# Optimization experiments

Hardware: AMD Instinct MI355X
Metric: run time of the kernel (lower is better)

## Reference

```python
import jax, jax.numpy as jnp
import numpy as np

N = 26000       # total nodes (1040 graphs * 25 joints)
E = 208000      # total edges
G = 1040        # graphs (16 samples * 65 frames)
FRAMES = 65
F_IN = 6
HID = 128
HEADS = 4
NCLS = 7


def setup_inputs() -> dict:
    key = jax.random.key(0)
    ks = jax.random.split(key, 30)

    def nrm(k, shape, s=0.05):
        return jax.random.normal(k, shape, dtype=jnp.float32) * s

    return {
        "x": jax.random.normal(ks[0], (N, F_IN), dtype=jnp.float32),
        "edge_index": jax.random.randint(ks[1], (2, E), 0, N, dtype=jnp.int32),
        "batch": jnp.arange(N, dtype=jnp.int32) // (N // G),  # 25 nodes per graph
        "w1_root": nrm(ks[2], (F_IN, HID)),
        "w1_nei": nrm(ks[3], (F_IN, HID)),
        "b1": nrm(ks[4], (HID,)),
        "wq": nrm(ks[5], (HID, HEADS * HID)),
        "bq": nrm(ks[6], (HEADS * HID,)),
        "wk": nrm(ks[7], (HID, HEADS * HID)),
        "bk": nrm(ks[8], (HEADS * HID,)),
        "wv": nrm(ks[9], (HID, HEADS * HID)),
        "bv": nrm(ks[10], (HEADS * HID,)),
        "wskip": nrm(ks[11], (HID, HEADS * HID)),
        "bskip": nrm(ks[12], (HEADS * HID,)),
        "skip_w": nrm(ks[13], (HID, HEADS * HID)),
        "lin1_w": nrm(ks[14], (HEADS * HID, HID)),
        "lin1_b": nrm(ks[15], (HID,)),
        "l2_root": nrm(ks[16], (HID, HID)),
        "l2_nei": nrm(ks[17], (HID, HID)),
        "l2_b": nrm(ks[18], (HID,)),
        "l3_root": nrm(ks[19], (HID, HID)),
        "l3_nei": nrm(ks[20], (HID, HID)),
        "l3_b": nrm(ks[21], (HID,)),
        "fc_w": nrm(ks[22], (HID, NCLS)),
        "fc_b": nrm(ks[23], (NCLS,)),
    }


def _graph_conv(x, src, dst, w_root, w_nei, b):
    # PyG GraphConv (aggr='add'): W_root x_i + W_nei * sum_{j in N(i)} x_j + b
    agg = jax.ops.segment_sum(x[src], dst, num_segments=N)
    return x @ w_root + agg @ w_nei + b


def _transformer_conv(x, src, dst, wq, bq, wk, bk, wv, bv, wskip, bskip):
    # PyG TransformerConv, concat=True, root_weight=True, beta=False.
    # Dropout on attention is inference-disabled.
    q = (x @ wq + bq).reshape(N, HEADS, HID)
    k = (x @ wk + bk).reshape(N, HEADS, HID)
    v = (x @ wv + bv).reshape(N, HEADS, HID)
    logits = jnp.einsum('ehc,ehc->eh', q[dst], k[src]) / jnp.sqrt(jnp.float32(HID))
    m = jax.ops.segment_max(logits, dst, num_segments=N)          # [N,H]
    a = jnp.exp(logits - m[dst])                                  # [E,H]
    denom = jax.ops.segment_sum(a, dst, num_segments=N)           # [N,H]
    num = jax.ops.segment_sum(a[:, :, None] * v[src], dst, num_segments=N)  # [N,H,C]
    out = num / jnp.where(denom == 0, 1.0, denom)[:, :, None]
    return out.reshape(N, HEADS * HID) + (x @ wskip + bskip)


def reference(x, edge_index, batch,
              w1_root, w1_nei, b1,
              wq, bq, wk, bk, wv, bv, wskip, bskip,
              skip_w, lin1_w, lin1_b,
              l2_root, l2_nei, l2_b,
              l3_root, l3_nei, l3_b,
              fc_w, fc_b):
    src, dst = edge_index[0], edge_index[1]
    h = jax.nn.relu(_graph_conv(x, src, dst, w1_root, w1_nei, b1))
    skip_out = h @ skip_w  # external skip Linear (no bias)
    h = jax.nn.relu(_transformer_conv(h, src, dst, wq, bq, wk, bk, wv, bv, wskip, bskip) + skip_out)
    h = jax.nn.relu(h @ lin1_w + lin1_b)
    for wr, wn, b in ((l2_root, l2_nei, l2_b), (l3_root, l3_nei, l3_b)):
        h = jax.nn.relu(_graph_conv(h, src, dst, wr, wn, b) + h)
    # global_mean_pool over graphs
    sums = jax.ops.segment_sum(h, batch, num_segments=G)
    cnts = jax.ops.segment_sum(jnp.ones((N,), jnp.float32), batch, num_segments=G)
    pooled = sums / jnp.where(cnts == 0, 1.0, cnts)[:, None]      # [G, HID]
    # average over 65 frames per sample, then classify
    z = pooled.reshape(-1, FRAMES, HID).mean(axis=1)              # [G/65, HID]
    return z @ fc_w + fc_b
```

## Files before the change

### kernel.cpp

```cpp
#include <hip/hip_runtime.h>
#include <math.h>

#define NN 26000
#define NE 208000
#define SCAN_CH 26
#define CNT_BLOCKS 813

typedef __attribute__((ext_vector_type(8))) short bf16x8;
typedef __attribute__((ext_vector_type(4))) float f32x4;
typedef __attribute__((ext_vector_type(2))) float f32x2;
typedef unsigned char u8;

__device__ __forceinline__ float bf2f(ushort u){
  union { unsigned int i; float f; } w; w.i = ((unsigned int)u) << 16; return w.f;
}
__device__ __forceinline__ ushort f2bf(float f){
  union { float f; unsigned int i; } w; w.f = f;
  unsigned int u = w.i + 0x7fffu + ((w.i >> 16) & 1u);
  return (ushort)(u >> 16);
}

__global__ void cp_k(const int* __restrict__ dst, int* __restrict__ cnt,
                     const float* __restrict__ wq, const float* __restrict__ wk,
                     const float* __restrict__ wv, const float* __restrict__ wskip,
                     const float* __restrict__ skw, const float* __restrict__ lin1w,
                     const float* __restrict__ l2r, const float* __restrict__ l2n,
                     const float* __restrict__ l3r, const float* __restrict__ l3n,
                     ushort* __restrict__ wbuf){
  if (blockIdx.x < CNT_BLOCKS){
    int e = blockIdx.x*256 + threadIdx.x;
    if (e < NE) atomicAdd(&cnt[dst[e]], 1);
    return;
  }
  int idx = (blockIdx.x - CNT_BLOCKS)*256 + threadIdx.x;
  if (idx >= 393216) return;
  float v;
  if (idx < 262144){
    int seg = idx >> 16;
    int local = idx & 65535;
    int n = local >> 7, kk = local & 127;
    const float* w = (seg == 0) ? wq : (seg == 1) ? wk : (seg == 2) ? wv : wskip;
    v = w[kk*512 + n];
    if (seg == 3) v += skw[kk*512 + n];
  } else if (idx < 327680){
    int local = idx - 262144;
    int n = local >> 9, kk = local & 511;
    v = lin1w[kk*128 + n];
  } else {
    int rem = idx - 327680;
    int seg = rem >> 14;
    int local = rem & 16383;
    int n = local >> 7, kk = local & 127;
    const float* w = (seg == 0) ? l2r : (seg == 1) ? l2n : (seg == 2) ? l3r : l3n;
    v = w[kk*128 + n];
  }
  wbuf[idx] = f2bf(v);
}

__global__ __launch_bounds__(1024) void scan_k(int* __restrict__ cnt_cur, int* __restrict__ off){
  int t = threadIdx.x;
  int base = t * SCAN_CH;
  int v[SCAN_CH];
  #pragma unroll
  for (int j = 0; j < SCAN_CH; ++j){
    int idx = base + j;
    v[j] = (idx < NN) ? cnt_cur[idx] : 0;
  }
  int s = 0;
  #pragma unroll
  for (int j = 0; j < SCAN_CH; ++j) s += v[j];
  __shared__ int ls[1024];
  ls[t] = s; __syncthreads();
  for (int ofs = 1; ofs < 1024; ofs <<= 1){
    int u = (t >= ofs) ? ls[t - ofs] : 0;
    __syncthreads();
    ls[t] += u;
    __syncthreads();
  }
  int run = (t == 0) ? 0 : ls[t-1];
  #pragma unroll
  for (int j = 0; j < SCAN_CH; ++j){
    int idx = base + j;
    if (idx < NN){
      off[idx] = run;
      cnt_cur[idx] = run;
      run += v[j];
    }
  }
  if (t == 1023) off[NN] = ls[1023];
}

__global__ void fill_k(const int* __restrict__ src, const int* __restrict__ dst,
                       int* __restrict__ cur, int* __restrict__ csrc, int E){
  int e = blockIdx.x*256 + threadIdx.x;
  if (e < E){
    int p = atomicAdd(&cur[dst[e]], 1);
    csrc[p] = src[e];
  }
}

__global__ __launch_bounds__(256) void layer1_k(
    const float* __restrict__ x, const int* __restrict__ off,
    const int* __restrict__ csrc, const float* __restrict__ w1r,
    const float* __restrict__ w1n, const float* __restrict__ b1,
    ushort* __restrict__ h1)
{
  __shared__ float aggs[2][6];
  int slot = threadIdx.x >> 7, c = threadIdx.x & 127;
  int i = blockIdx.x*2 + slot;
  if (c < 6){
    float s = 0.f;
    int e1 = off[i+1];
    for (int j = off[i]; j < e1; ++j) s += x[(size_t)csrc[j]*6 + c];
    aggs[slot][c] = s;
  }
  __syncthreads();
  float s = b1[c];
  #pragma unroll
  for (int f = 0; f < 6; ++f){
    s = fmaf(x[i*6+f],    w1r[f*128+c], s);
    s = fmaf(aggs[slot][f], w1n[f*128+c], s);
  }
  h1[(size_t)i*128 + c] = f2bf(fmaxf(s, 0.f));
}

__global__ __launch_bounds__(256) void qkvs_k(
    const ushort* __restrict__ A, const ushort* __restrict__ BT,
    const float* __restrict__ bq, const float* __restrict__ bk,
    const float* __restrict__ bv, const float* __restrict__ bs,
    u8* __restrict__ cq, u8* __restrict__ ckv,
    ushort* __restrict__ cs, int M)
{
  __shared__ ushort smem[2*128*72];
  ushort* Asm = smem;
  ushort* Bsm = smem + 128*72;
  int tid  = threadIdx.x;
  int lane = tid & 63;
  int wid  = tid >> 6;
  int wr = wid >> 1, wc = wid & 1;
  int rowbase = blockIdx.y * 128;
  int seg = blockIdx.x >> 2;
  const float* bias = (seg == 0) ? bq : (seg == 1) ? bk : (seg == 2) ? bv : bs;
  int colloc = (blockIdx.x & 3) * 128;
  int lr = lane & 15, lk = (lane >> 4) * 8;

  f32x4 acc[4][4] = {};

  for (int k0 = 0; k0 < 128; k0 += 64){
    #pragma unroll
    for (int i = 0; i < 4; ++i){
      int c = tid + i*256;
      int r = c >> 3, col8 = (c & 7) * 8;
      int row = rowbase + r;
      bf16x8 av = (bf16x8)0;
      if (row < M) av = *reinterpret_cast<const bf16x8*>(A + (size_t)row*128 + k0 + col8);
      *reinterpret_cast<bf16x8*>(&Asm[r*72 + col8]) = av;
      *reinterpret_cast<bf16x8*>(&Bsm[r*72 + col8]) =
          *reinterpret_cast<const bf16x8*>(BT + (size_t)(blockIdx.x*128 + r)*128 + k0 + col8);
    }
    __syncthreads();
    #pragma unroll
    for (int ks = 0; ks < 64; ks += 32){
      bf16x8 af[4], bfr[4];
      #pragma unroll
      for (int i = 0; i < 4; ++i)
        af[i] = *reinterpret_cast<const bf16x8*>(&Asm[(wr*64 + i*16 + lr)*72 + ks + lk]);
      #pragma unroll
      for (int j = 0; j < 4; ++j)
        bfr[j] = *reinterpret_cast<const bf16x8*>(&Bsm[(wc*64 + j*16 + lr)*72 + ks + lk]);
      #pragma unroll
      for (int i = 0; i < 4; ++i)
        #pragma unroll
        for (int j = 0; j < 4; ++j)
          acc[i][j] = __builtin_amdgcn_mfma_f32_16x16x32_bf16(af[i], bfr[j], acc[i][j], 0, 0, 0);
    }
    __syncthreads();
  }

  int rq = lane >> 4;
  #pragma unroll
  for (int i = 0; i < 4; ++i)
    #pragma unroll
    for (int r = 0; r < 4; ++r){
      int lrow = wr*64 + i*16 + rq*4 + r;
      #pragma unroll
      for (int j = 0; j < 4; ++j){
        int lcol = wc*64 + j*16 + lr;
        smem[lrow*136 + lcol] = f2bf(acc[i][j][r] + bias[colloc + lcol]);
      }
    }
  __syncthreads();

  if (seg <= 2){
    u8* Cb; int ldb, cb;
    if (seg == 0){ Cb = cq;  ldb = 512;  cb = colloc; }
    else         { Cb = ckv; ldb = 1024; cb = (seg == 1 ? 0 : 512) + colloc; }
    #pragma unroll
    for (int t = tid; t < 2048; t += 256){
      int r = t >> 4, s8 = (t & 15) * 8;
      int row = rowbase + r;
      if (row < M){
        bf16x8 hv = *reinterpret_cast<const bf16x8*>(&smem[r*136 + s8]);
        unsigned int lo = 0, hi = 0;
        lo = __builtin_amdgcn_cvt_pk_fp8_f32(bf2f((ushort)hv[0]), bf2f((ushort)hv[1]), lo, false);
        lo = __builtin_amdgcn_cvt_pk_fp8_f32(bf2f((ushort)hv[2]), bf2f((ushort)hv[3]), lo, true);
        hi = __builtin_amdgcn_cvt_pk_fp8_f32(bf2f((ushort)hv[4]), bf2f((ushort)hv[5]), hi, false);
        hi = __builtin_amdgcn_cvt_pk_fp8_f32(bf2f((ushort)hv[6]), bf2f((ushort)hv[7]), hi, true);
        uint2 o; o.x = lo; o.y = hi;
        *reinterpret_cast<uint2*>(Cb + (size_t)row*ldb + cb + s8) = o;
      }
    }
  } else {
    #pragma unroll
    for (int t = tid; t < 2048; t += 256){
      int r = t >> 4, s8 = (t & 15) * 8;
      int row = rowbase + r;
      if (row < M)
        *reinterpret_cast<bf16x8*>(cs + (size_t)row*512 + colloc + s8) =
            *reinterpret_cast<const bf16x8*>(&smem[r*136 + s8]);
    }
  }
}

__global__ __launch_bounds__(256) void bgemm64_k(
    const ushort* __restrict__ A1, int lda1, const ushort* __restrict__ B1T, int K1,
    const float* __restrict__ bias, ushort* __restrict__ C, int M, int N)
{
  __shared__ ushort As[64][72];
  __shared__ ushort Bs[128][72];
  int tid  = threadIdx.x;
  int lane = tid & 63;
  int wid  = tid >> 6;
  int wr = wid >> 1, wc = wid & 1;
  int rowbase = blockIdx.y * 64;
  int colbase = blockIdx.x * 128;
  int lr = lane & 15, lk = (lane >> 4) * 8;

  f32x4 acc[2][4] = {};

  for (int k0 = 0; k0 < K1; k0 += 64){
    #pragma unroll
    for (int i = 0; i < 2; ++i){
      int c = tid + i*256;
      int r = c >> 3, col8 = (c & 7) * 8;
      int row = rowbase + r;
      bf16x8 av = (bf16x8)0;
      if (row < M) av = *reinterpret_cast<const bf16x8*>(A1 + (size_t)row*lda1 + k0 + col8);
      *reinterpret_cast<bf16x8*>(&As[r][col8]) = av;
    }
    #pragma unroll
    for (int i = 0; i < 4; ++i){
      int c = tid + i*256;
      int r = c >> 3, col8 = (c & 7) * 8;
      *reinterpret_cast<bf16x8*>(&Bs[r][col8]) =
          *reinterpret_cast<const bf16x8*>(B1T + (size_t)(colbase + r)*K1 + k0 + col8);
    }
    __syncthreads();
    #pragma unroll
    for (int ks = 0; ks < 64; ks += 32){
      bf16x8 af[2], bfr[4];
      #pragma unroll
      for (int i = 0; i < 2; ++i)
        af[i] = *reinterpret_cast<const bf16x8*>(&As[wr*32 + i*16 + lr][ks + lk]);
      #pragma unroll
      for (int j = 0; j < 4; ++j)
        bfr[j] = *reinterpret_cast<const bf16x8*>(&Bs[wc*64 + j*16 + lr][ks + lk]);
      #pragma unroll
      for (int i = 0; i < 2; ++i)
        #pragma unroll
        for (int j = 0; j < 4; ++j)
          acc[i][j] = __builtin_amdgcn_mfma_f32_16x16x32_bf16(af[i], bfr[j], acc[i][j], 0, 0, 0);
    }
    __syncthreads();
  }

  int rq = lane >> 4;
  #pragma unroll
  for (int i = 0; i < 2; ++i){
    #pragma unroll
    for (int r = 0; r < 4; ++r){
      int row = rowbase + wr*32 + i*16 + rq*4 + r;
      if (row >= M) continue;
      #pragma unroll
      for (int j = 0; j < 4; ++j){
        int col = colbase + wc*64 + j*16 + lr;
        if (col >= N) continue;
        float v = fmaxf(acc[i][j][r] + bias[col], 0.f);
        C[(size_t)row*N + col] = f2bf(v);
      }
    }
  }
}

__global__ __launch_bounds__(256) void gconv_k(
    const ushort* __restrict__ h, const ushort* __restrict__ WrT,
    const ushort* __restrict__ WnT, const float* __restrict__ bias,
    const int* __restrict__ off, const int* __restrict__ csrc,
    ushort* __restrict__ out, int M)
{
  __shared__ ushort As1[64][136];
  __shared__ ushort As2[64][136];
  int tid = threadIdx.x, lane = tid & 63, wid = tid >> 6;
  int wr = wid >> 1, wc = wid & 1;
  int rowbase = blockIdx.x * 64;
  int lr = lane & 15, lk = (lane >> 4) * 8;

  #pragma unroll
  for (int it = 0; it < 4; ++it){
    int c = tid + it*256;
    int r = c >> 4, col8 = (c & 15) * 8;
    int row = rowbase + r;
    bf16x8 av = (bf16x8)0;
    if (row < M) av = *reinterpret_cast<const bf16x8*>(h + (size_t)row*128 + col8);
    *reinterpret_cast<bf16x8*>(&As1[r][col8]) = av;
  }
  {
    int r = tid >> 2, sl = tid & 3;
    int row = rowbase + r;
    float a[32] = {};
    if (row < M){
      int e1 = off[row+1];
      for (int j = off[row]; j < e1; ++j){
        const ushort* hp = h + (size_t)csrc[j]*128 + sl*32;
        #pragma unroll
        for (int u = 0; u < 4; ++u){
          bf16x8 hv = *reinterpret_cast<const bf16x8*>(hp + u*8);
          #pragma unroll
          for (int p = 0; p < 8; ++p) a[u*8+p] += bf2f((ushort)hv[p]);
        }
      }
    }
    #pragma unroll
    for (int u = 0; u < 4; ++u){
      bf16x8 o;
      #pragma unroll
      for (int p = 0; p < 8; ++p) o[p] = (short)f2bf(a[u*8+p]);
      *reinterpret_cast<bf16x8*>(&As2[r][sl*32 + u*8]) = o;
    }
  }
  __syncthreads();

  f32x4 acc[2][4] = {};
  #pragma unroll
  for (int pass = 0; pass < 2; ++pass){
    const ushort* BT = pass ? WnT : WrT;
    #pragma unroll
    for (int kk = 0; kk < 128; kk += 32){
      bf16x8 af[2], bfr[4];
      #pragma unroll
      for (int i = 0; i < 2; ++i)
        af[i] = pass
          ? *reinterpret_cast<const bf16x8*>(&As2[wr*32 + i*16 + lr][kk + lk])
          : *reinterpret_cast<const bf16x8*>(&As1[wr*32 + i*16 + lr][kk + lk]);
      #pragma unroll
      for (int j = 0; j < 4; ++j)
        bfr[j] = *reinterpret_cast<const bf16x8*>(
            BT + (size_t)(wc*64 + j*16 + lr)*128 + kk + lk);
      #pragma unroll
      for (int i = 0; i < 2; ++i)
        #pragma unroll
        for (int j = 0; j < 4; ++j)
          acc[i][j] = __builtin_amdgcn_mfma_f32_16x16x32_bf16(af[i], bfr[j], acc[i][j], 0, 0, 0);
    }
  }

  int rq = lane >> 4;
  #pragma unroll
  for (int i = 0; i < 2; ++i){
    #pragma unroll
    for (int r = 0; r < 4; ++r){
      int lrow = wr*32 + i*16 + rq*4 + r;
      int row = rowbase + lrow;
      if (row >= M) continue;
      #pragma unroll
      for (int j = 0; j < 4; ++j){
        int col = wc*64 + j*16 + lr;
        float v = acc[i][j][r] + bias[col] + bf2f(As1[lrow][col]);
        out[(size_t)row*128 + col] = f2bf(fmaxf(v, 0.f));
      }
    }
  }
}

__global__ __launch_bounds__(256) void attn_k(
    const u8* __restrict__ q, const u8* __restrict__ kv,
    ushort* __restrict__ s_io,
    const int* __restrict__ off, const int* __restrict__ csrc)
{
  int lane = threadIdx.x & 63;
  int i = blockIdx.x*4 + (threadIdx.x >> 6);
  uint2 qv = *reinterpret_cast<const uint2*>(q + (size_t)i*512 + lane*8);
  f32x2 q01 = __builtin_amdgcn_cvt_pk_f32_fp8(qv.x, false);
  f32x2 q23 = __builtin_amdgcn_cvt_pk_f32_fp8(qv.x, true);
  f32x2 q45 = __builtin_amdgcn_cvt_pk_f32_fp8(qv.y, false);
  f32x2 q67 = __builtin_amdgcn_cvt_pk_f32_fp8(qv.y, true);
  float qf[8] = {q01[0], q01[1], q23[0], q23[1], q45[0], q45[1], q67[0], q67[1]};

  float d = 0.f, acc[8] = {};
  int e0 = off[i], e1 = off[i+1];
  uint2 kA, vA, kB, vB;
  if (e0 < e1){
    const u8* r = kv + (size_t)csrc[e0]*1024 + lane*8;
    kA = *reinterpret_cast<const uint2*>(r);
    vA = *reinterpret_cast<const uint2*>(r + 512);
  }
  if (e0 + 1 < e1){
    const u8* r = kv + (size_t)csrc[e0+1]*1024 + lane*8;
    kB = *reinterpret_cast<const uint2*>(r);
    vB = *reinterpret_cast<const uint2*>(r + 512);
  }
  for (int j = e0; j < e1; ++j){
    uint2 kc = kA, vc = vA;
    kA = kB; vA = vB;
    if (j + 2 < e1){
      const u8* r = kv + (size_t)csrc[j+2]*1024 + lane*8;
      kB = *reinterpret_cast<const uint2*>(r);
      vB = *reinterpret_cast<const uint2*>(r + 512);
    }
    f32x2 k01 = __builtin_amdgcn_cvt_pk_f32_fp8(kc.x, false);
    f32x2 k23 = __builtin_amdgcn_cvt_pk_f32_fp8(kc.x, true);
    f32x2 k45 = __builtin_amdgcn_cvt_pk_f32_fp8(kc.y, false);
    f32x2 k67 = __builtin_amdgcn_cvt_pk_f32_fp8(kc.y, true);
    float t;
    t = qf[0] * k01[0];
    t = fmaf(qf[1], k01[1], t);
    t = fmaf(qf[2], k23[0], t);
    t = fmaf(qf[3], k23[1], t);
    t = fmaf(qf[4], k45[0], t);
    t = fmaf(qf[5], k45[1], t);
    t = fmaf(qf[6], k67[0], t);
    t = fmaf(qf[7], k67[1], t);
    t += __shfl_xor(t, 1);
    t += __shfl_xor(t, 2);
    t += __shfl_xor(t, 4);
    t += __shfl_xor(t, 8);
    float w = __expf(t * 0.08838834764831845f);
    d += w;
    f32x2 v01 = __builtin_amdgcn_cvt_pk_f32_fp8(vc.x, false);
    f32x2 v23 = __builtin_amdgcn_cvt_pk_f32_fp8(vc.x, true);
    f32x2 v45 = __builtin_amdgcn_cvt_pk_f32_fp8(vc.y, false);
    f32x2 v67 = __builtin_amdgcn_cvt_pk_f32_fp8(vc.y, true);
    acc[0] = fmaf(w, v01[0], acc[0]);
    acc[1] = fmaf(w, v01[1], acc[1]);
    acc[2] = fmaf(w, v23[0], acc[2]);
    acc[3] = fmaf(w, v23[1], acc[3]);
    acc[4] = fmaf(w, v45[0], acc[4]);
    acc[5] = fmaf(w, v45[1], acc[5]);
    acc[6] = fmaf(w, v67[0], acc[6]);
    acc[7] = fmaf(w, v67[1], acc[7]);
  }
  float inv = (d > 0.f) ? 1.f/d : 0.f;
  ushort* rowp = s_io + (size_t)i*512 + lane*8;
  bf16x8 sk8 = *reinterpret_cast<const bf16x8*>(rowp);
  bf16x8 o8;
  #pragma unroll
  for (int p = 0; p < 8; ++p)
    o8[p] = (short)f2bf(fmaxf(bf2f((ushort)sk8[p]) + acc[p]*inv, 0.f));
  *reinterpret_cast<bf16x8*>(rowp) = o8;
}

__global__ __launch_bounds__(256) void fc1_k(const ushort* __restrict__ h,
                                             float* __restrict__ partial){
  int s = blockIdx.x, c0 = blockIdx.y;
  int t = threadIdx.x;
  int c = t & 127, g = t >> 7;
  float sum = 0.f;
  int rend = (c0 + 1) * 125;
  for (int r = c0*125 + g; r < rend; r += 2)
    sum += bf2f(h[((size_t)s*1625 + r)*128 + c]);
  __shared__ float zs[2][128];
  zs[g][c] = sum; __syncthreads();
  if (g == 0) partial[((size_t)s*13 + c0)*128 + c] = zs[0][c] + zs[1][c];
}

__global__ __launch_bounds__(128) void fc2_k(const float* __restrict__ partial,
    const float* __restrict__ fcw, const float* __restrict__ fcb,
    float* __restrict__ out)
{
  int s = blockIdx.x;
  int c = threadIdx.x;
  float z = 0.f;
  #pragma unroll
  for (int p = 0; p < 13; ++p) z += partial[((size_t)s*13 + p)*128 + c];
  __shared__ float zs[128];
  zs[c] = z * (1.0f/1625.0f);
  __syncthreads();
  if (c < 7){
    float o = fcb[c];
    for (int k2 = 0; k2 < 128; ++k2) o = fmaf(zs[k2], fcw[k2*7 + c], o);
    out[s*7 + c] = o;
  }
}

extern "C" void kernel_launch(void* const* d_in, const int* in_sizes, int n_in,
                              void* d_out, int out_size, void* d_ws, size_t ws_size,
                              hipStream_t stream)
{
  const float* x     = (const float*)d_in[0];
  const int*   ei    = (const int*)  d_in[1];
  const float* w1r   = (const float*)d_in[3];
  const float* w1n   = (const float*)d_in[4];
  const float* b1    = (const float*)d_in[5];
  const float* wq    = (const float*)d_in[6];
  const float* bq    = (const float*)d_in[7];
  const float* wk    = (const float*)d_in[8];
  const float* bk    = (const float*)d_in[9];
  const float* wv    = (const float*)d_in[10];
  const float* bv    = (const float*)d_in[11];
  const float* wskip = (const float*)d_in[12];
  const float* bskip = (const float*)d_in[13];
  const float* skw   = (const float*)d_in[14];
  const float* lin1w = (const float*)d_in[15];
  const float* lin1b = (const float*)d_in[16];
  const float* l2r   = (const float*)d_in[17];
  const float* l2n   = (const float*)d_in[18];
  const float* l2b   = (const float*)d_in[19];
  const float* l3r   = (const float*)d_in[20];
  const float* l3n   = (const float*)d_in[21];
  const float* l3b   = (const float*)d_in[22];
  const float* fcw   = (const float*)d_in[23];
  const float* fcb   = (const float*)d_in[24];
  float* out = (float*)d_out;

  const int* src = ei;
  const int* dst = ei + NE;

  char* base = (char*)d_ws;
  size_t o = 0;
  auto alloc = [&](size_t bytes) -> void* {
    o = (o + 255) & ~(size_t)255;
    void* p = base + o; o += bytes; return p;
  };
  int*    cnt     = (int*)   alloc((size_t)NN*4);
  int*    off     = (int*)   alloc((size_t)(NN+1)*4);
  int*    csrc    = (int*)   alloc((size_t)NE*4);
  float*  partial = (float*) alloc((size_t)16*13*128*4);
  ushort* h1      = (ushort*)alloc((size_t)NN*128*2);
  ushort* wbuf    = (ushort*)alloc((size_t)393216*2);
  u8*     bufQ8   = (u8*)    alloc((size_t)NN*512);
  u8*     bufKV   = (u8*)    alloc((size_t)NN*1024);
  ushort* bufS    = (ushort*)alloc((size_t)NN*512*2);
  ushort* hbuf    = (ushort*)alloc((size_t)NN*256*2);
  (void)ws_size; (void)in_sizes; (void)n_in; (void)out_size;

  const ushort* lin1T = wbuf + 262144;
  const ushort* l2rT  = wbuf + 327680;
  const ushort* l2nT  = wbuf + 344064;
  const ushort* l3rT  = wbuf + 360448;
  const ushort* l3nT  = wbuf + 376832;

  ushort* h3 = hbuf;
  ushort* h4 = hbuf + (size_t)NN*128;
  ushort* h5 = bufS;

  hipMemsetAsync(cnt, 0, (size_t)NN*4, stream);
  cp_k<<<CNT_BLOCKS + 1536, 256, 0, stream>>>(dst, cnt,
      wq, wk, wv, wskip, skw, lin1w, l2r, l2n, l3r, l3n, wbuf);
  scan_k<<<1, 1024, 0, stream>>>(cnt, off);
  fill_k<<<(NE+255)/256, 256, 0, stream>>>(src, dst, cnt, csrc, NE);

  layer1_k<<<NN/2, 256, 0, stream>>>(x, off, csrc, w1r, w1n, b1, h1);

  {
    dim3 g(16, (NN+127)/128);
    qkvs_k<<<g, 256, 0, stream>>>(h1, wbuf, bq, bk, bv, bskip,
                                  bufQ8, bufKV, bufS, NN);
  }

  attn_k<<<NN/4, 256, 0, stream>>>(bufQ8, bufKV, bufS, off, csrc);

  {
    dim3 g(1, (NN+63)/64);
    bgemm64_k<<<g, 256, 0, stream>>>(bufS, 512, lin1T, 512, lin1b, h3, NN, 128);
  }

  gconv_k<<<(NN+63)/64, 256, 0, stream>>>(h3, l2rT, l2nT, l2b, off, csrc, h4, NN);
  gconv_k<<<(NN+63)/64, 256, 0, stream>>>(h4, l3rT, l3nT, l3b, off, csrc, h5, NN);

  {
    dim3 g1(16, 13);
    fc1_k<<<g1, 256, 0, stream>>>(h5, partial);
    fc2_k<<<16, 128, 0, stream>>>(partial, fcw, fcb, out);
  }
}
```

Before: 287.6 us.

## Reuse A tile across four column tiles in QKVS GEMM, load B from global

The QKVS projection kernel now loads the full 128x128 A tile into shared memory once per block and loops over four 128-column output tiles, so the grid shrinks from 16 to 4 column blocks. This cuts the redundant reloads of A. B fragments are read directly from global memory (L2/L1) instead of being staged in LDS. The epilogue is split into two 64-row halves through a smaller staging buffer, and the launch bounds request 3 blocks per CU. The costs are fewer blocks and therefore less parallelism, uncoalesced-ish direct global B loads in the inner loop, and extra barriers in the epilogue.

```diff
diff --git a/kernel.cpp b/kernel.cpp
--- a/kernel.cpp
+++ b/kernel.cpp
@@ -124,100 +124,101 @@
   h1[(size_t)i*128 + c] = f2bf(fmaxf(s, 0.f));
 }
 
-__global__ __launch_bounds__(256) void qkvs_k(
+__global__ __launch_bounds__(256, 3) void qkvs_k(
     const ushort* __restrict__ A, const ushort* __restrict__ BT,
     const float* __restrict__ bq, const float* __restrict__ bk,
     const float* __restrict__ bv, const float* __restrict__ bs,
     u8* __restrict__ cq, u8* __restrict__ ckv,
     ushort* __restrict__ cs, int M)
 {
-  __shared__ ushort smem[2*128*72];
-  ushort* Asm = smem;
-  ushort* Bsm = smem + 128*72;
-  int tid  = threadIdx.x;
-  int lane = tid & 63;
-  int wid  = tid >> 6;
+  __shared__ ushort Asm[128*136];
+  __shared__ ushort epi[64*136];
+  int tid = threadIdx.x;
+  int lane = tid & 63, wid = tid >> 6;
   int wr = wid >> 1, wc = wid & 1;
+  int seg = blockIdx.x;
   int rowbase = blockIdx.y * 128;
-  int seg = blockIdx.x >> 2;
   const float* bias = (seg == 0) ? bq : (seg == 1) ? bk : (seg == 2) ? bv : bs;
-  int colloc = (blockIdx.x & 3) * 128;
   int lr = lane & 15, lk = (lane >> 4) * 8;
-
-  f32x4 acc[4][4] = {};
-
-  for (int k0 = 0; k0 < 128; k0 += 64){
-    #pragma unroll
-    for (int i = 0; i < 4; ++i){
-      int c = tid + i*256;
-      int r = c >> 3, col8 = (c & 7) * 8;
-      int row = rowbase + r;
-      bf16x8 av = (bf16x8)0;
-      if (row < M) av = *reinterpret_cast<const bf16x8*>(A + (size_t)row*128 + k0 + col8);
-      *reinterpret_cast<bf16x8*>(&Asm[r*72 + col8]) = av;
-      *reinterpret_cast<bf16x8*>(&Bsm[r*72 + col8]) =
-          *reinterpret_cast<const bf16x8*>(BT + (size_t)(blockIdx.x*128 + r)*128 + k0 + col8);
-    }
-    __syncthreads();
-    #pragma unroll
-    for (int ks = 0; ks < 64; ks += 32){
+  int rq = lane >> 4;
+
+  #pragma unroll
+  for (int it = 0; it < 8; ++it){
+    int c = tid + it*256;
+    int r = c >> 4, col8 = (c & 15) * 8;
+    int row = rowbase + r;
+    bf16x8 av = (bf16x8)0;
+    if (row < M) av = *reinterpret_cast<const bf16x8*>(A + (size_t)row*128 + col8);
+    *reinterpret_cast<bf16x8*>(&Asm[r*136 + col8]) = av;
+  }
+  __syncthreads();
+
+  for (int ct = 0; ct < 4; ++ct){
+    int colloc = ct * 128;
+    f32x4 acc[4][4] = {};
+    #pragma unroll
+    for (int kk = 0; kk < 128; kk += 32){
       bf16x8 af[4], bfr[4];
       #pragma unroll
       for (int i = 0; i < 4; ++i)
-        af[i] = *reinterpret_cast<const bf16x8*>(&Asm[(wr*64 + i*16 + lr)*72 + ks + lk]);
+        af[i] = *reinterpret_cast<const bf16x8*>(&Asm[(wr*64 + i*16 + lr)*136 + kk + lk]);
       #pragma unroll
       for (int j = 0; j < 4; ++j)
-        bfr[j] = *reinterpret_cast<const bf16x8*>(&Bsm[(wc*64 + j*16 + lr)*72 + ks + lk]);
+        bfr[j] = *reinterpret_cast<const bf16x8*>(
+            BT + (size_t)(seg*512 + colloc + wc*64 + j*16 + lr)*128 + kk + lk);
       #pragma unroll
       for (int i = 0; i < 4; ++i)
         #pragma unroll
         for (int j = 0; j < 4; ++j)
           acc[i][j] = __builtin_amdgcn_mfma_f32_16x16x32_bf16(af[i], bfr[j], acc[i][j], 0, 0, 0);
     }
-    __syncthreads();
-  }
-
-  int rq = lane >> 4;
-  #pragma unroll
-  for (int i = 0; i < 4; ++i)
-    #pragma unroll
-    for (int r = 0; r < 4; ++r){
-      int lrow = wr*64 + i*16 + rq*4 + r;
-      #pragma unroll
-      for (int j = 0; j < 4; ++j){
-        int lcol = wc*64 + j*16 + lr;
-        smem[lrow*136 + lcol] = f2bf(acc[i][j][r] + bias[colloc + lcol]);
+
+    #pragma unroll
+    for (int p = 0; p < 2; ++p){
+      __syncthreads();
+      if (wr == p){
+        #pragma unroll
+        for (int i = 0; i < 4; ++i)
+          #pragma unroll
+          for (int r = 0; r < 4; ++r){
+            int lrow = i*16 + rq*4 + r;
+            #pragma unroll
+            for (int j = 0; j < 4; ++j){
+              int lcol = wc*64 + j*16 + lr;
+              epi[lrow*136 + lcol] = f2bf(acc[i][j][r] + bias[colloc + lcol]);
+            }
+          }
       }
-    }
-  __syncthreads();
-
-  if (seg <= 2){
-    u8* Cb; int ldb, cb;
-    if (seg == 0){ Cb = cq;  ldb = 512;  cb = colloc; }
-    else         { Cb = ckv; ldb = 1024; cb = (seg == 1 ? 0 : 512) + colloc; }
-    #pragma unroll
-    for (int t = tid; t < 2048; t += 256){
-      int r = t >> 4, s8 = (t & 15) * 8;
-      int row = rowbase + r;
-      if (row < M){
-        bf16x8 hv = *reinterpret_cast<const bf16x8*>(&smem[r*136 + s8]);
-        unsigned int lo = 0, hi = 0;
-        lo = __builtin_amdgcn_cvt_pk_fp8_f32(bf2f((ushort)hv[0]), bf2f((ushort)hv[1]), lo, false);
-        lo = __builtin_amdgcn_cvt_pk_fp8_f32(bf2f((ushort)hv[2]), bf2f((ushort)hv[3]), lo, true);
-        hi = __builtin_amdgcn_cvt_pk_fp8_f32(bf2f((ushort)hv[4]), bf2f((ushort)hv[5]), hi, false);
-        hi = __builtin_amdgcn_cvt_pk_fp8_f32(bf2f((ushort)hv[6]), bf2f((ushort)hv[7]), hi, true);
-        uint2 o; o.x = lo; o.y = hi;
-        *reinterpret_cast<uint2*>(Cb + (size_t)row*ldb + cb + s8) = o;
+      __syncthreads();
+      if (seg <= 2){
+        u8* Cb; int ldb, cb;
+        if (seg == 0){ Cb = cq;  ldb = 512;  cb = colloc; }
+        else         { Cb = ckv; ldb = 1024; cb = (seg == 1 ? 0 : 512) + colloc; }
+        #pragma unroll
+        for (int t = tid; t < 1024; t += 256){
+          int r = t >> 4, s8 = (t & 15) * 8;
+          int row = rowbase + p*64 + r;
+          if (row < M){
+            bf16x8 hv = *reinterpret_cast<const bf16x8*>(&epi[r*136 + s8]);
+            unsigned int lo = 0, hi = 0;
+            lo = __builtin_amdgcn_cvt_pk_fp8_f32(bf2f((ushort)hv[0]), bf2f((ushort)hv[1]), lo, false);
+            lo = __builtin_amdgcn_cvt_pk_fp8_f32(bf2f((ushort)hv[2]), bf2f((ushort)hv[3]), lo, true);
+            hi = __builtin_amdgcn_cvt_pk_fp8_f32(bf2f((ushort)hv[4]), bf2f((ushort)hv[5]), hi, false);
+            hi = __builtin_amdgcn_cvt_pk_fp8_f32(bf2f((ushort)hv[6]), bf2f((ushort)hv[7]), hi, true);
+            uint2 o; o.x = lo; o.y = hi;
+            *reinterpret_cast<uint2*>(Cb + (size_t)row*ldb + cb + s8) = o;
+          }
+        }
+      } else {
+        #pragma unroll
+        for (int t = tid; t < 1024; t += 256){
+          int r = t >> 4, s8 = (t & 15) * 8;
+          int row = rowbase + p*64 + r;
+          if (row < M)
+            *reinterpret_cast<bf16x8*>(cs + (size_t)row*512 + colloc + s8) =
+                *reinterpret_cast<const bf16x8*>(&epi[r*136 + s8]);
+        }
       }
-    }
-  } else {
-    #pragma unroll
-    for (int t = tid; t < 2048; t += 256){
-      int r = t >> 4, s8 = (t & 15) * 8;
-      int row = rowbase + r;
-      if (row < M)
-        *reinterpret_cast<bf16x8*>(cs + (size_t)row*512 + colloc + s8) =
-            *reinterpret_cast<const bf16x8*>(&smem[r*136 + s8]);
     }
   }
 }
@@ -562,7 +563,7 @@
   layer1_k<<<NN/2, 256, 0, stream>>>(x, off, csrc, w1r, w1n, b1, h1);
 
   {
-    dim3 g(16, (NN+127)/128);
+    dim3 g(4, (NN+127)/128);
     qkvs_k<<<g, 256, 0, stream>>>(h1, wbuf, bq, bk, bv, bskip,
                                   bufQ8, bufKV, bufS, NN);
   }
```

New measurement: 311.2 us. 1.08x slower.

## Refactor attention algebraically: fold Wk into query side and apply Wv after aggregation

Applied to the files above, without the earlier changes.

Precomputes Wq·Wk^T per head and bq·Wk^T, so each node's query is projected into the 128-dim input space (u). Attention logits then become dot products of u with raw fp8 neighbour features h1 instead of gathered K rows, which shrinks per-edge gather traffic from 1 KB of K/V per edge to 128 bytes of h1. The key bias is dropped, which is exact because it adds the same constant to every logit of a destination node and cancels in the softmax. Values are aggregated in input space and the V projection is applied afterwards by a separate MFMA GEMM kernel, with bv scaled by a has-neighbours flag. This adds a kernel launch and a large bf16 aggregation buffer, and the fp8 quantisation of h1 and u may shift accuracy.

```diff
diff --git a/kernel.cpp b/kernel.cpp
--- a/kernel.cpp
+++ b/kernel.cpp
@@ -22,39 +22,67 @@
 
 __global__ void cp_k(const int* __restrict__ dst, int* __restrict__ cnt,
                      const float* __restrict__ wq, const float* __restrict__ wk,
-                     const float* __restrict__ wv, const float* __restrict__ wskip,
-                     const float* __restrict__ skw, const float* __restrict__ lin1w,
+                     const float* __restrict__ wv, const float* __restrict__ bq,
+                     const float* __restrict__ wskip, const float* __restrict__ skw,
+                     const float* __restrict__ lin1w,
                      const float* __restrict__ l2r, const float* __restrict__ l2n,
                      const float* __restrict__ l3r, const float* __restrict__ l3n,
-                     ushort* __restrict__ wbuf){
-  if (blockIdx.x < CNT_BLOCKS){
-    int e = blockIdx.x*256 + threadIdx.x;
+                     ushort* __restrict__ wbuf, float* __restrict__ bu){
+  int b = blockIdx.x, t = threadIdx.x;
+  if (b < CNT_BLOCKS){
+    int e = b*256 + t;
     if (e < NE) atomicAdd(&cnt[dst[e]], 1);
     return;
   }
-  int idx = (blockIdx.x - CNT_BLOCKS)*256 + threadIdx.x;
-  if (idx >= 393216) return;
-  float v;
-  if (idx < 262144){
-    int seg = idx >> 16;
-    int local = idx & 65535;
-    int n = local >> 7, kk = local & 127;
-    const float* w = (seg == 0) ? wq : (seg == 1) ? wk : (seg == 2) ? wv : wskip;
-    v = w[kk*512 + n];
-    if (seg == 3) v += skw[kk*512 + n];
-  } else if (idx < 327680){
-    int local = idx - 262144;
-    int n = local >> 9, kk = local & 511;
-    v = lin1w[kk*128 + n];
-  } else {
-    int rem = idx - 327680;
-    int seg = rem >> 14;
-    int local = rem & 16383;
-    int n = local >> 7, kk = local & 127;
-    const float* w = (seg == 0) ? l2r : (seg == 1) ? l2n : (seg == 2) ? l3r : l3n;
-    v = w[kk*128 + n];
-  }
-  wbuf[idx] = f2bf(v);
+  b -= CNT_BLOCKS;
+  if (b < 256){
+    int idx = b*256 + t;
+    int n = idx >> 7, k2 = idx & 127, h = n >> 7, m = n & 127;
+    const float* wqr = wq + (size_t)k2*512 + h*128;
+    const float* wkr = wk + (size_t)m*512 + h*128;
+    float s = 0.f;
+    for (int c = 0; c < 128; ++c) s = fmaf(wqr[c], wkr[c], s);
+    wbuf[idx] = f2bf(s);
+    return;
+  }
+  b -= 256;
+  if (b < 2){
+    int n = b*256 + t;
+    int h = n >> 7, m = n & 127;
+    const float* wkr = wk + (size_t)m*512 + h*128;
+    float s = 0.f;
+    for (int c = 0; c < 128; ++c) s = fmaf(bq[h*128 + c], wkr[c], s);
+    bu[n] = s;
+    return;
+  }
+  b -= 2;
+  if (b < 256){
+    int idx = b*256 + t;
+    int n = idx >> 7, m = idx & 127;
+    wbuf[196608 + idx] = f2bf(wv[(size_t)m*512 + n]);
+    return;
+  }
+  b -= 256;
+  if (b < 256){
+    int idx = b*256 + t;
+    int n = idx >> 7, k2 = idx & 127;
+    wbuf[65536 + idx] = f2bf(wskip[(size_t)k2*512 + n] + skw[(size_t)k2*512 + n]);
+    return;
+  }
+  b -= 256;
+  if (b < 256){
+    int idx = b*256 + t;
+    int n = idx >> 9, k2 = idx & 511;
+    wbuf[131072 + idx] = f2bf(lin1w[(size_t)k2*128 + n]);
+    return;
+  }
+  b -= 256;
+  {
+    int idx = b*256 + t;
+    int sg = idx >> 14, loc = idx & 16383, n = loc >> 7, k2 = loc & 127;
+    const float* w = (sg == 0) ? l2r : (sg == 1) ? l2n : (sg == 2) ? l3r : l3n;
+    wbuf[262144 + idx] = f2bf(w[(size_t)k2*128 + n]);
+  }
 }
 
 __global__ __launch_bounds__(1024) void scan_k(int* __restrict__ cnt_cur, int* __restrict__ off){
@@ -103,7 +131,7 @@
     const float* __restrict__ x, const int* __restrict__ off,
     const int* __restrict__ csrc, const float* __restrict__ w1r,
     const float* __restrict__ w1n, const float* __restrict__ b1,
-    ushort* __restrict__ h1)
+    ushort* __restrict__ h1, u8* __restrict__ h1f)
 {
   __shared__ float aggs[2][6];
   int slot = threadIdx.x >> 7, c = threadIdx.x & 127;
@@ -121,15 +149,16 @@
     s = fmaf(x[i*6+f],    w1r[f*128+c], s);
     s = fmaf(aggs[slot][f], w1n[f*128+c], s);
   }
-  h1[(size_t)i*128 + c] = f2bf(fmaxf(s, 0.f));
-}
-
-__global__ __launch_bounds__(256) void qkvs_k(
-    const ushort* __restrict__ A, const ushort* __restrict__ BT,
-    const float* __restrict__ bq, const float* __restrict__ bk,
-    const float* __restrict__ bv, const float* __restrict__ bs,
-    u8* __restrict__ cq, u8* __restrict__ ckv,
-    ushort* __restrict__ cs, int M)
+  float r = fmaxf(s, 0.f);
+  h1[(size_t)i*128 + c] = f2bf(r);
+  unsigned int pk = __builtin_amdgcn_cvt_pk_fp8_f32(r, r, 0u, false);
+  h1f[(size_t)i*128 + c] = (u8)(pk & 0xffu);
+}
+
+__global__ __launch_bounds__(256) void us_k(
+    const ushort* __restrict__ A, const ushort* __restrict__ wbuf,
+    const float* __restrict__ bu, const float* __restrict__ bskip,
+    u8* __restrict__ cu, ushort* __restrict__ cs, int M)
 {
   __shared__ ushort smem[2*128*72];
   ushort* Asm = smem;
@@ -140,8 +169,9 @@
   int wr = wid >> 1, wc = wid & 1;
   int rowbase = blockIdx.y * 128;
   int seg = blockIdx.x >> 2;
-  const float* bias = (seg == 0) ? bq : (seg == 1) ? bk : (seg == 2) ? bv : bs;
   int colloc = (blockIdx.x & 3) * 128;
+  const ushort* BT = wbuf + (seg ? 65536 : 0);
+  const float* bias = seg ? bskip : bu;
   int lr = lane & 15, lk = (lane >> 4) * 8;
 
   f32x4 acc[4][4] = {};
@@ -156,7 +186,7 @@
       if (row < M) av = *reinterpret_cast<const bf16x8*>(A + (size_t)row*128 + k0 + col8);
       *reinterpret_cast<bf16x8*>(&Asm[r*72 + col8]) = av;
       *reinterpret_cast<bf16x8*>(&Bsm[r*72 + col8]) =
-          *reinterpret_cast<const bf16x8*>(BT + (size_t)(blockIdx.x*128 + r)*128 + k0 + col8);
+          *reinterpret_cast<const bf16x8*>(BT + (size_t)(colloc + r)*128 + k0 + col8);
     }
     __syncthreads();
     #pragma unroll
@@ -191,10 +221,7 @@
     }
   __syncthreads();
 
-  if (seg <= 2){
-    u8* Cb; int ldb, cb;
-    if (seg == 0){ Cb = cq;  ldb = 512;  cb = colloc; }
-    else         { Cb = ckv; ldb = 1024; cb = (seg == 1 ? 0 : 512) + colloc; }
+  if (seg == 0){
     #pragma unroll
     for (int t = tid; t < 2048; t += 256){
       int r = t >> 4, s8 = (t & 15) * 8;
@@ -207,7 +234,7 @@
         hi = __builtin_amdgcn_cvt_pk_fp8_f32(bf2f((ushort)hv[4]), bf2f((ushort)hv[5]), hi, false);
         hi = __builtin_amdgcn_cvt_pk_fp8_f32(bf2f((ushort)hv[6]), bf2f((ushort)hv[7]), hi, true);
         uint2 o; o.x = lo; o.y = hi;
-        *reinterpret_cast<uint2*>(Cb + (size_t)row*ldb + cb + s8) = o;
+        *reinterpret_cast<uint2*>(cu + (size_t)row*512 + colloc + s8) = o;
       }
     }
   } else {
@@ -218,6 +245,147 @@
       if (row < M)
         *reinterpret_cast<bf16x8*>(cs + (size_t)row*512 + colloc + s8) =
             *reinterpret_cast<const bf16x8*>(&smem[r*136 + s8]);
+    }
+  }
+}
+
+__global__ __launch_bounds__(256) void attn_k(
+    const u8* __restrict__ u, const u8* __restrict__ h1f,
+    ushort* __restrict__ aggout, float* __restrict__ beta,
+    const int* __restrict__ off, const int* __restrict__ csrc)
+{
+  int lane = threadIdx.x & 63;
+  int i = blockIdx.x*4 + (threadIdx.x >> 6);
+  int cb = 2*lane;
+  float uf[4][2];
+  #pragma unroll
+  for (int h = 0; h < 4; ++h){
+    ushort uu = *reinterpret_cast<const ushort*>(u + (size_t)i*512 + h*128 + cb);
+    f32x2 p = __builtin_amdgcn_cvt_pk_f32_fp8((unsigned int)uu, false);
+    uf[h][0] = p[0]; uf[h][1] = p[1];
+  }
+  float d[4] = {0,0,0,0}, agg[4][2] = {};
+  int e0 = off[i], e1 = off[i+1];
+  ushort hA = 0, hB = 0;
+  if (e0 < e1)     hA = *reinterpret_cast<const ushort*>(h1f + (size_t)csrc[e0]*128 + cb);
+  if (e0 + 1 < e1) hB = *reinterpret_cast<const ushort*>(h1f + (size_t)csrc[e0+1]*128 + cb);
+  for (int j = e0; j < e1; ++j){
+    ushort hc = hA; hA = hB;
+    if (j + 2 < e1) hB = *reinterpret_cast<const ushort*>(h1f + (size_t)csrc[j+2]*128 + cb);
+    f32x2 hj = __builtin_amdgcn_cvt_pk_f32_fp8((unsigned int)hc, false);
+    float p0 = fmaf(uf[0][1], hj[1], uf[0][0]*hj[0]);
+    float p1 = fmaf(uf[1][1], hj[1], uf[1][0]*hj[0]);
+    float p2 = fmaf(uf[2][1], hj[1], uf[2][0]*hj[0]);
+    float p3 = fmaf(uf[3][1], hj[1], uf[3][0]*hj[0]);
+    #pragma unroll
+    for (int o = 32; o; o >>= 1){
+      p0 += __shfl_xor(p0, o);
+      p1 += __shfl_xor(p1, o);
+      p2 += __shfl_xor(p2, o);
+      p3 += __shfl_xor(p3, o);
+    }
+    const float sc = 0.08838834764831845f;
+    float a0 = __expf(p0*sc), a1 = __expf(p1*sc), a2 = __expf(p2*sc), a3 = __expf(p3*sc);
+    d[0] += a0; d[1] += a1; d[2] += a2; d[3] += a3;
+    agg[0][0] = fmaf(a0, hj[0], agg[0][0]); agg[0][1] = fmaf(a0, hj[1], agg[0][1]);
+    agg[1][0] = fmaf(a1, hj[0], agg[1][0]); agg[1][1] = fmaf(a1, hj[1], agg[1][1]);
+    agg[2][0] = fmaf(a2, hj[0], agg[2][0]); agg[2][1] = fmaf(a2, hj[1], agg[2][1]);
+    agg[3][0] = fmaf(a3, hj[0], agg[3][0]); agg[3][1] = fmaf(a3, hj[1], agg[3][1]);
+  }
+  #pragma unroll
+  for (int h = 0; h < 4; ++h){
+    float inv = (d[h] > 0.f) ? 1.f/d[h] : 0.f;
+    ushort2 o;
+    o.x = f2bf(agg[h][0]*inv);
+    o.y = f2bf(agg[h][1]*inv);
+    *reinterpret_cast<ushort2*>(aggout + (size_t)i*512 + h*128 + cb) = o;
+  }
+  if (lane == 0){
+    #pragma unroll
+    for (int h = 0; h < 4; ++h) beta[i*4 + h] = (d[h] > 0.f) ? 1.f : 0.f;
+  }
+}
+
+__global__ __launch_bounds__(256) void vproj_k(
+    const ushort* __restrict__ agg, const ushort* __restrict__ vT,
+    const float* __restrict__ bv, const float* __restrict__ beta,
+    ushort* __restrict__ s_io, int M)
+{
+  __shared__ ushort smem[2*128*72];
+  __shared__ float sbeta[128];
+  ushort* Asm = smem;
+  ushort* Bsm = smem + 128*72;
+  int tid = threadIdx.x;
+  int lane = tid & 63, wid = tid >> 6;
+  int wr = wid >> 1, wc = wid & 1;
+  int seg = blockIdx.x;
+  int rowbase = blockIdx.y * 128;
+  int lr = lane & 15, lk = (lane >> 4) * 8;
+  int rq = lane >> 4;
+
+  if (tid < 128){
+    int row = rowbase + tid;
+    sbeta[tid] = (row < M) ? beta[row*4 + seg] : 0.f;
+  }
+
+  f32x4 acc[4][4] = {};
+  for (int k0 = 0; k0 < 128; k0 += 64){
+    #pragma unroll
+    for (int i = 0; i < 4; ++i){
+      int c = tid + i*256;
+      int r = c >> 3, col8 = (c & 7) * 8;
+      int row = rowbase + r;
+      bf16x8 av = (bf16x8)0;
+      if (row < M) av = *reinterpret_cast<const bf16x8*>(agg + (size_t)row*512 + seg*128 + k0 + col8);
+      *reinterpret_cast<bf16x8*>(&Asm[r*72 + col8]) = av;
+      *reinterpret_cast<bf16x8*>(&Bsm[r*72 + col8]) =
+          *reinterpret_cast<const bf16x8*>(vT + (size_t)(seg*128 + r)*128 + k0 + col8);
+    }
+    __syncthreads();
+    #pragma unroll
+    for (int ks = 0; ks < 64; ks += 32){
+      bf16x8 af[4], bfr[4];
+      #pragma unroll
+      for (int i = 0; i < 4; ++i)
+        af[i] = *reinterpret_cast<const bf16x8*>(&Asm[(wr*64 + i*16 + lr)*72 + ks + lk]);
+      #pragma unroll
+      for (int j = 0; j < 4; ++j)
+        bfr[j] = *reinterpret_cast<const bf16x8*>(&Bsm[(wc*64 + j*16 + lr)*72 + ks + lk]);
+      #pragma unroll
+      for (int i = 0; i < 4; ++i)
+        #pragma unroll
+        for (int j = 0; j < 4; ++j)
+          acc[i][j] = __builtin_amdgcn_mfma_f32_16x16x32_bf16(af[i], bfr[j], acc[i][j], 0, 0, 0);
+    }
+    __syncthreads();
+  }
+
+  #pragma unroll
+  for (int i = 0; i < 4; ++i)
+    #pragma unroll
+    for (int r = 0; r < 4; ++r){
+      int lrow = wr*64 + i*16 + rq*4 + r;
+      #pragma unroll
+      for (int j = 0; j < 4; ++j){
+        int lcol = wc*64 + j*16 + lr;
+        float v = acc[i][j][r] + bv[seg*128 + lcol] * sbeta[lrow];
+        smem[lrow*136 + lcol] = f2bf(v);
+      }
+    }
+  __syncthreads();
+  #pragma unroll
+  for (int t = tid; t < 2048; t += 256){
+    int r = t >> 4, s8 = (t & 15) * 8;
+    int row = rowbase + r;
+    if (row < M){
+      ushort* p = s_io + (size_t)row*512 + seg*128 + s8;
+      bf16x8 sv = *reinterpret_cast<const bf16x8*>(p);
+      bf16x8 tv = *reinterpret_cast<const bf16x8*>(&smem[r*136 + s8]);
+      bf16x8 o;
+      #pragma unroll
+      for (int q2 = 0; q2 < 8; ++q2)
+        o[q2] = (short)f2bf(fmaxf(bf2f((ushort)sv[q2]) + bf2f((ushort)tv[q2]), 0.f));
+      *reinterpret_cast<bf16x8*>(p) = o;
     }
   }
 }
@@ -382,83 +550,6 @@
   }
 }
 
-__global__ __launch_bounds__(256) void attn_k(
-    const u8* __restrict__ q, const u8* __restrict__ kv,
-    ushort* __restrict__ s_io,
-    const int* __restrict__ off, const int* __restrict__ csrc)
-{
-  int lane = threadIdx.x & 63;
-  int i = blockIdx.x*4 + (threadIdx.x >> 6);
-  uint2 qv = *reinterpret_cast<const uint2*>(q + (size_t)i*512 + lane*8);
-  f32x2 q01 = __builtin_amdgcn_cvt_pk_f32_fp8(qv.x, false);
-  f32x2 q23 = __builtin_amdgcn_cvt_pk_f32_fp8(qv.x, true);
-  f32x2 q45 = __builtin_amdgcn_cvt_pk_f32_fp8(qv.y, false);
-  f32x2 q67 = __builtin_amdgcn_cvt_pk_f32_fp8(qv.y, true);
-  float qf[8] = {q01[0], q01[1], q23[0], q23[1], q45[0], q45[1], q67[0], q67[1]};
-
-  float d = 0.f, acc[8] = {};
-  int e0 = off[i], e1 = off[i+1];
-  uint2 kA, vA, kB, vB;
-  if (e0 < e1){
-    const u8* r = kv + (size_t)csrc[e0]*1024 + lane*8;
-    kA = *reinterpret_cast<const uint2*>(r);
-    vA = *reinterpret_cast<const uint2*>(r + 512);
-  }
-  if (e0 + 1 < e1){
-    const u8* r = kv + (size_t)csrc[e0+1]*1024 + lane*8;
-    kB = *reinterpret_cast<const uint2*>(r);
-    vB = *reinterpret_cast<const uint2*>(r + 512);
-  }
-  for (int j = e0; j < e1; ++j){
-    uint2 kc = kA, vc = vA;
-    kA = kB; vA = vB;
-    if (j + 2 < e1){
-      const u8* r = kv + (size_t)csrc[j+2]*1024 + lane*8;
-      kB = *reinterpret_cast<const uint2*>(r);
-      vB = *reinterpret_cast<const uint2*>(r + 512);
-    }
-    f32x2 k01 = __builtin_amdgcn_cvt_pk_f32_fp8(kc.x, false);
-    f32x2 k23 = __builtin_amdgcn_cvt_pk_f32_fp8(kc.x, true);
-    f32x2 k45 = __builtin_amdgcn_cvt_pk_f32_fp8(kc.y, false);
-    f32x2 k67 = __builtin_amdgcn_cvt_pk_f32_fp8(kc.y, true);
-    float t;
-    t = qf[0] * k01[0];
-    t = fmaf(qf[1], k01[1], t);
-    t = fmaf(qf[2], k23[0], t);
-    t = fmaf(qf[3], k23[1], t);
-    t = fmaf(qf[4], k45[0], t);
-    t = fmaf(qf[5], k45[1], t);
-    t = fmaf(qf[6], k67[0], t);
-    t = fmaf(qf[7], k67[1], t);
-    t += __shfl_xor(t, 1);
-    t += __shfl_xor(t, 2);
-    t += __shfl_xor(t, 4);
-    t += __shfl_xor(t, 8);
-    float w = __expf(t * 0.08838834764831845f);
-    d += w;
-    f32x2 v01 = __builtin_amdgcn_cvt_pk_f32_fp8(vc.x, false);
-    f32x2 v23 = __builtin_amdgcn_cvt_pk_f32_fp8(vc.x, true);
-    f32x2 v45 = __builtin_amdgcn_cvt_pk_f32_fp8(vc.y, false);
-    f32x2 v67 = __builtin_amdgcn_cvt_pk_f32_fp8(vc.y, true);
-    acc[0] = fmaf(w, v01[0], acc[0]);
-    acc[1] = fmaf(w, v01[1], acc[1]);
-    acc[2] = fmaf(w, v23[0], acc[2]);
-    acc[3] = fmaf(w, v23[1], acc[3]);
-    acc[4] = fmaf(w, v45[0], acc[4]);
-    acc[5] = fmaf(w, v45[1], acc[5]);
-    acc[6] = fmaf(w, v67[0], acc[6]);
-    acc[7] = fmaf(w, v67[1], acc[7]);
-  }
-  float inv = (d > 0.f) ? 1.f/d : 0.f;
-  ushort* rowp = s_io + (size_t)i*512 + lane*8;
-  bf16x8 sk8 = *reinterpret_cast<const bf16x8*>(rowp);
-  bf16x8 o8;
-  #pragma unroll
-  for (int p = 0; p < 8; ++p)
-    o8[p] = (short)f2bf(fmaxf(bf2f((ushort)sk8[p]) + acc[p]*inv, 0.f));
-  *reinterpret_cast<bf16x8*>(rowp) = o8;
-}
-
 __global__ __launch_bounds__(256) void fc1_k(const ushort* __restrict__ h,
                                              float* __restrict__ partial){
   int s = blockIdx.x, c0 = blockIdx.y;
@@ -504,7 +595,6 @@
   const float* wq    = (const float*)d_in[6];
   const float* bq    = (const float*)d_in[7];
   const float* wk    = (const float*)d_in[8];
-  const float* bk    = (const float*)d_in[9];
   const float* wv    = (const float*)d_in[10];
   const float* bv    = (const float*)d_in[11];
   const float* wskip = (const float*)d_in[12];
@@ -535,39 +625,47 @@
   int*    off     = (int*)   alloc((size_t)(NN+1)*4);
   int*    csrc    = (int*)   alloc((size_t)NE*4);
   float*  partial = (float*) alloc((size_t)16*13*128*4);
+  float*  bu      = (float*) alloc((size_t)512*4);
+  float*  beta    = (float*) alloc((size_t)NN*4*4);
   ushort* h1      = (ushort*)alloc((size_t)NN*128*2);
-  ushort* wbuf    = (ushort*)alloc((size_t)393216*2);
-  u8*     bufQ8   = (u8*)    alloc((size_t)NN*512);
-  u8*     bufKV   = (u8*)    alloc((size_t)NN*1024);
+  u8*     h1f     = (u8*)    alloc((size_t)NN*128);
+  ushort* wbuf    = (ushort*)alloc((size_t)327680*2);
+  u8*     bufU8   = (u8*)    alloc((size_t)NN*512);
+  ushort* aggbuf  = (ushort*)alloc((size_t)NN*512*2);
   ushort* bufS    = (ushort*)alloc((size_t)NN*512*2);
   ushort* hbuf    = (ushort*)alloc((size_t)NN*256*2);
   (void)ws_size; (void)in_sizes; (void)n_in; (void)out_size;
 
-  const ushort* lin1T = wbuf + 262144;
-  const ushort* l2rT  = wbuf + 327680;
-  const ushort* l2nT  = wbuf + 344064;
-  const ushort* l3rT  = wbuf + 360448;
-  const ushort* l3nT  = wbuf + 376832;
+  const ushort* lin1T = wbuf + 131072;
+  const ushort* vT    = wbuf + 196608;
+  const ushort* l2rT  = wbuf + 262144;
+  const ushort* l2nT  = wbuf + 278528;
+  const ushort* l3rT  = wbuf + 294912;
+  const ushort* l3nT  = wbuf + 311296;
 
   ushort* h3 = hbuf;
   ushort* h4 = hbuf + (size_t)NN*128;
   ushort* h5 = bufS;
 
   hipMemsetAsync(cnt, 0, (size_t)NN*4, stream);
-  cp_k<<<CNT_BLOCKS + 1536, 256, 0, stream>>>(dst, cnt,
-      wq, wk, wv, wskip, skw, lin1w, l2r, l2n, l3r, l3n, wbuf);
+  cp_k<<<CNT_BLOCKS + 256 + 2 + 256 + 256 + 256 + 256, 256, 0, stream>>>(
+      dst, cnt, wq, wk, wv, bq, wskip, skw, lin1w, l2r, l2n, l3r, l3n, wbuf, bu);
   scan_k<<<1, 1024, 0, stream>>>(cnt, off);
   fill_k<<<(NE+255)/256, 256, 0, stream>>>(src, dst, cnt, csrc, NE);
 
-  layer1_k<<<NN/2, 256, 0, stream>>>(x, off, csrc, w1r, w1n, b1, h1);
+  layer1_k<<<NN/2, 256, 0, stream>>>(x, off, csrc, w1r, w1n, b1, h1, h1f);
 
   {
-    dim3 g(16, (NN+127)/128);
-    qkvs_k<<<g, 256, 0, stream>>>(h1, wbuf, bq, bk, bv, bskip,
-                                  bufQ8, bufKV, bufS, NN);
-  }
-
-  attn_k<<<NN/4, 256, 0, stream>>>(bufQ8, bufKV, bufS, off, csrc);
+    dim3 g(8, (NN+127)/128);
+    us_k<<<g, 256, 0, stream>>>(h1, wbuf, bu, bskip, bufU8, bufS, NN);
+  }
+
+  attn_k<<<NN/4, 256, 0, stream>>>(bufU8, h1f, aggbuf, beta, off, csrc);
+
+  {
+    dim3 g(4, (NN+127)/128);
+    vproj_k<<<g, 256, 0, stream>>>(aggbuf, vT, bv, beta, bufS, NN);
+  }
 
   {
     dim3 g(1, (NN+63)/64);
```

New measurement: 324.8 us. 12.9% more time.
